# Optimization experiments

Measured on AMD Instinct MI355X. Metric: run time of the kernel, lower is better.

## Reference

```python
import jax, jax.numpy as jnp
import numpy as np

N = 100_000   # nodes
E = 1_600_000 # edges (avg degree 16)
B = 512       # graphs in batch
F_IN = 64; H = 4; D = 64; HD = H * D; EXTRA = 16
NEG_SLOPE = 0.2  # DGL GATConv default


def _gat_conv(x, src, dst, W, al, ar, bias):
    """DGL GATConv: fc -> per-head attn logits -> edge leaky_relu -> segment softmax over dst -> scatter-sum."""
    h = (x @ W).reshape(N, H, D)                       # [N,H,D]
    el = jnp.sum(h * al, axis=-1)                      # [N,H]
    er = jnp.sum(h * ar, axis=-1)                      # [N,H]
    e = jax.nn.leaky_relu(el[src] + er[dst], NEG_SLOPE)  # [E,H]
    m = jax.ops.segment_max(e, dst, num_segments=N)    # [N,H]
    m = jnp.where(jnp.isfinite(m), m, 0.0)             # guard empty segments
    ex = jnp.exp(e - m[dst])                           # [E,H]
    den = jax.ops.segment_sum(ex, dst, num_segments=N) # [N,H]
    alpha = ex / jnp.maximum(den[dst], 1e-9)           # [E,H]
    msg = h[src] * alpha[:, :, None]                   # [E,H,D]
    out = jax.ops.segment_sum(msg, dst, num_segments=N) + bias.reshape(1, H, D)
    return out  # [N,H,D]


def setup_inputs() -> dict:
    key = jax.random.key(0)
    ks = jax.random.split(key, 26)
    nrm = lambda k, shape: jax.random.normal(k, shape, dtype=jnp.float32) * 0.5
    src = jax.random.randint(ks[0], (E,), 0, N)
    # ensure every node has >=1 incoming edge (DGL disallows zero in-degree by default)
    dst = jnp.concatenate([jnp.arange(N), jax.random.randint(ks[1], (E - N,), 0, N)])
    node_graph = jnp.sort(jax.random.randint(ks[2], (N,), 0, B))
    inp = dict(
        src=src, dst=dst, node_graph=node_graph,
        feats_node=jax.random.normal(ks[3], (N, F_IN), dtype=jnp.float32),
        feats_graph=jax.random.normal(ks[4], (B, EXTRA), dtype=jnp.float32),
        W1=nrm(ks[5], (F_IN, HD)), al1=nrm(ks[6], (H, D)), ar1=nrm(ks[7], (H, D)), bg1=jnp.zeros(HD),
        W2=nrm(ks[8], (HD, HD)),  al2=nrm(ks[9], (H, D)), ar2=nrm(ks[10], (H, D)), bg2=jnp.zeros(HD),
        W3=nrm(ks[11], (HD, HD)), al3=nrm(ks[12], (H, D)), ar3=nrm(ks[13], (H, D)), bg3=jnp.zeros(HD),
        sw=nrm(ks[14], (HD, 1)), sb=jnp.zeros(1),
        lw1=nrm(ks[15], (HD + EXTRA, 2 * D)), lb1=jnp.zeros(2 * D),
        lw2=nrm(ks[16], (2 * D, D)), lb2=jnp.zeros(D),
        lw3=nrm(ks[17], (D, 1)), lb3=jnp.zeros(1),
    )
    return inp


def reference(src, dst, node_graph, feats_node, feats_graph,
              W1, al1, ar1, bg1, W2, al2, ar2, bg2, W3, al3, ar3, bg3,
              sw, sb, lw1, lb1, lw2, lb2, lw3, lb3):
    selu = jax.nn.selu
    x = selu(_gat_conv(feats_node, src, dst, W1, al1, ar1, bg1)).reshape(N, HD)
    x = selu(_gat_conv(x, src, dst, W2, al2, ar2, bg2)).reshape(N, HD)
    x = selu(_gat_conv(x, src, dst, W3, al3, ar3, bg3)).reshape(N, HD)
    # WeightedAverage readout: sigmoid-scored weighted mean per graph
    w = jax.nn.sigmoid(x @ sw + sb)                               # [N,1]
    num = jax.ops.segment_sum(w * x, node_graph, num_segments=B)  # [B,HD]
    den = jax.ops.segment_sum(w, node_graph, num_segments=B)      # [B,1]
    emb = num / jnp.maximum(den, 1e-9)
    y = jnp.concatenate([emb, feats_graph], axis=1)
    y = selu(y @ lw1 + lb1)
    y = selu(y @ lw2 + lb2)
    return y @ lw3 + lb3  # [B,1]
```

## Files before the change

kernel.cpp:

```cpp
#include <hip/hip_runtime.h>

#define N_NODES 100000
#define N_EDGES 1600000
#define N_GRAPHS 512
#define F_IN 64
#define HD 256
#define EXTRA 16
#define SCAN_BLOCK 512

typedef float f32x4 __attribute__((ext_vector_type(4)));
typedef _Float16 f16x4 __attribute__((ext_vector_type(4)));
typedef _Float16 f16x8 __attribute__((ext_vector_type(8)));

__device__ __forceinline__ float selu_f(float x) {
    const float a = 1.6732632423543772f, sc = 1.0507009873554805f;
    return x > 0.f ? sc * x : sc * a * (__expf(x) - 1.f);
}

__global__ __launch_bounds__(256) void hist_k(const int* __restrict__ dst, int* __restrict__ hist) {
    int j = blockIdx.x * 256 + threadIdx.x;
    if (j < N_EDGES) atomicAdd(&hist[dst[j]], 1);
}

__global__ __launch_bounds__(SCAN_BLOCK) void scan1_k(const int* __restrict__ hist,
                                                      int* __restrict__ row_ptr,
                                                      int* __restrict__ bsums) {
    __shared__ int sm[SCAN_BLOCK];
    int t = threadIdx.x;
    int i = blockIdx.x * SCAN_BLOCK + t;
    int v = (i < N_NODES) ? hist[i] : 0;
    sm[t] = v;
    __syncthreads();
    for (int off = 1; off < SCAN_BLOCK; off <<= 1) {
        int add = (t >= off) ? sm[t - off] : 0;
        __syncthreads();
        sm[t] += add;
        __syncthreads();
    }
    if (i < N_NODES) row_ptr[i] = sm[t] - v;
    if (t == SCAN_BLOCK - 1) bsums[blockIdx.x] = sm[t];
}

__global__ __launch_bounds__(256) void scan23_k(int* __restrict__ row_ptr, const int* __restrict__ bsums,
                                                int* __restrict__ cursor, int nb) {
    __shared__ int bs[256];
    int t = threadIdx.x;
    bs[t] = (t < nb) ? bsums[t] : 0;
    __syncthreads();
    for (int off = 1; off < 256; off <<= 1) {
        int add = (t >= off) ? bs[t - off] : 0;
        __syncthreads();
        bs[t] += add;
        __syncthreads();
    }
    int i = blockIdx.x * 256 + t;
    if (i < N_NODES) {
        int b = i / SCAN_BLOCK;
        int p = b > 0 ? bs[b - 1] : 0;
        int r = row_ptr[i] + p;
        row_ptr[i] = r;
        cursor[i] = r;
    }
    if (i == 0) row_ptr[N_NODES] = N_EDGES;
}

__global__ __launch_bounds__(256) void scatter_k(const int* __restrict__ src,
                                                 const int* __restrict__ dst,
                                                 int* __restrict__ cursor,
                                                 int* __restrict__ csr_src) {
    int j = blockIdx.x * 256 + threadIdx.x;
    if (j < N_EDGES) {
        int r = atomicAdd(&cursor[dst[j]], 1);
        csr_src[r] = src[j];
    }
}

__device__ __forceinline__ void wsplit(const float* __restrict__ W, _Float16* __restrict__ Wh,
                                       _Float16* __restrict__ Wl, int idx, int K) {
    int n = idx / K, k = idx - n * K;
    float w = W[(size_t)k * HD + n];
    _Float16 hi = (_Float16)w;
    Wh[idx] = hi;
    Wl[idx] = (_Float16)(w - (float)hi);
}

__global__ __launch_bounds__(256) void prep_k(const float* __restrict__ W1,
                                              const float* __restrict__ W2,
                                              const float* __restrict__ W3,
                                              _Float16* __restrict__ W1h, _Float16* __restrict__ W1l,
                                              _Float16* __restrict__ W2h, _Float16* __restrict__ W2l,
                                              _Float16* __restrict__ W3h, _Float16* __restrict__ W3l,
                                              const int* __restrict__ node_graph,
                                              int* __restrict__ gstart) {
    int b = blockIdx.x, t = threadIdx.x;
    if (b < 64) {
        wsplit(W1, W1h, W1l, b * 256 + t, F_IN);
    } else if (b < 320) {
        wsplit(W2, W2h, W2l, (b - 64) * 256 + t, HD);
    } else if (b < 576) {
        wsplit(W3, W3h, W3l, (b - 320) * 256 + t, HD);
    } else {
        int g = (b - 576) * 256 + t;
        if (g > N_GRAPHS) return;
        int lo = 0, hi = N_NODES;
        while (lo < hi) {
            int mid = (lo + hi) >> 1;
            if (node_graph[mid] < g) lo = mid + 1; else hi = mid;
        }
        gstart[g] = lo;
    }
}

template <int K, bool F32A>
__global__ __launch_bounds__(256) void gemm_split_k(const void* __restrict__ Aptr,
                                                    const _Float16* __restrict__ Alo_p,
                                                    const _Float16* __restrict__ Bt_hi,
                                                    const _Float16* __restrict__ Bt_lo,
                                                    const float* __restrict__ al,
                                                    const float* __restrict__ ar,
                                                    _Float16* __restrict__ Chi,
                                                    float* __restrict__ el,
                                                    float* __restrict__ er, int M) {
    const int BM = 64, BN = 128, LDP = 40;
    __shared__ union {
        struct {
            _Float16 Ash[BM][LDP];
            _Float16 Asl[BM][LDP];
            _Float16 Bsh[BN][LDP];
            _Float16 Bsl[BN][LDP];
        } s;
        _Float16 ctile[BM][BN];
    } u;
    __shared__ float pl[4][64];
    __shared__ float pr[4][64];
    _Float16 (&Ash)[BM][LDP] = u.s.Ash;
    _Float16 (&Asl)[BM][LDP] = u.s.Asl;
    _Float16 (&Bsh)[BN][LDP] = u.s.Bsh;
    _Float16 (&Bsl)[BN][LDP] = u.s.Bsl;

    int tid = threadIdx.x;
    int w = tid >> 6, lane = tid & 63;
    int q = lane >> 4, l16 = lane & 15;
    int row0 = blockIdx.y * BM, col0 = blockIdx.x * BN;
    f32x4 acc[4][2] = {};

    int ar_ = tid >> 2, ao = (tid & 3) * 8;
    f16x8 rAh, rAl, rBh[2], rBl[2];

    auto load_tile = [&](int k0) {
        int gr = row0 + ar_;
        if constexpr (F32A) {
            const float* A32 = (const float*)Aptr;
            float vv[8] = {};
            if (gr < M) {
                float4 va = *(const float4*)(A32 + (size_t)gr * K + k0 + ao);
                float4 vb = *(const float4*)(A32 + (size_t)gr * K + k0 + ao + 4);
                vv[0] = va.x; vv[1] = va.y; vv[2] = va.z; vv[3] = va.w;
                vv[4] = vb.x; vv[5] = vb.y; vv[6] = vb.z; vv[7] = vb.w;
            }
            f16x8 h, l;
#pragma unroll
            for (int i = 0; i < 8; i++) {
                h[i] = (_Float16)vv[i];
                l[i] = (_Float16)(vv[i] - (float)h[i]);
            }
            rAh = h; rAl = l;
        } else {
            const _Float16* Ahi = (const _Float16*)Aptr;
            f16x8 vh = {}, vl = {};
            if (gr < M) {
                vh = *(const f16x8*)(Ahi + (size_t)gr * K + k0 + ao);
                vl = *(const f16x8*)(Alo_p + (size_t)gr * K + k0 + ao);
            }
            rAh = vh; rAl = vl;
        }
#pragma unroll
        for (int c = 0; c < 2; c++) {
            int cc = tid + c * 256;
            int br = cc >> 2, bo = (cc & 3) * 8;
            int gb = col0 + br;
            rBh[c] = *(const f16x8*)(Bt_hi + (size_t)gb * K + k0 + bo);
            rBl[c] = *(const f16x8*)(Bt_lo + (size_t)gb * K + k0 + bo);
        }
    };
    auto store_tile = [&]() {
        *(f16x8*)&Ash[ar_][ao] = rAh;
        *(f16x8*)&Asl[ar_][ao] = rAl;
#pragma unroll
        for (int c = 0; c < 2; c++) {
            int cc = tid + c * 256;
            int br = cc >> 2, bo = (cc & 3) * 8;
            *(f16x8*)&Bsh[br][bo] = rBh[c];
            *(f16x8*)&Bsl[br][bo] = rBl[c];
        }
    };

    load_tile(0);
    store_tile();
    __syncthreads();

    for (int k0 = 0; k0 < K; k0 += 32) {
        bool more = (k0 + 32) < K;
        if (more) load_tile(k0 + 32);

        f16x8 ah[4], alo2[4], bh[2], bl[2];
#pragma unroll
        for (int mf = 0; mf < 4; mf++) {
            int m = mf * 16 + l16;
            ah[mf] = *(const f16x8*)&Ash[m][q * 8];
            alo2[mf] = *(const f16x8*)&Asl[m][q * 8];
        }
#pragma unroll
        for (int nf = 0; nf < 2; nf++) {
            int n = w * 32 + nf * 16 + l16;
            bh[nf] = *(const f16x8*)&Bsh[n][q * 8];
            bl[nf] = *(const f16x8*)&Bsl[n][q * 8];
        }
#pragma unroll
        for (int mf = 0; mf < 4; mf++)
#pragma unroll
            for (int nf = 0; nf < 2; nf++) {
                acc[mf][nf] = __builtin_amdgcn_mfma_f32_16x16x32_f16(ah[mf], bh[nf], acc[mf][nf], 0, 0, 0);
                acc[mf][nf] = __builtin_amdgcn_mfma_f32_16x16x32_f16(ah[mf], bl[nf], acc[mf][nf], 0, 0, 0);
                acc[mf][nf] = __builtin_amdgcn_mfma_f32_16x16x32_f16(alo2[mf], bh[nf], acc[mf][nf], 0, 0, 0);
            }
        if (more) {
            __syncthreads();
            store_tile();
            __syncthreads();
        }
    }

    __syncthreads();

    const int hh = (col0 >> 6) + (w >> 1);
    float alv[2], arv[2];
#pragma unroll
    for (int nf = 0; nf < 2; nf++) {
        int d = (w & 1) * 32 + nf * 16 + l16;
        alv[nf] = al[hh * 64 + d];
        arv[nf] = ar[hh * 64 + d];
    }
#pragma unroll
    for (int mf = 0; mf < 4; mf++) {
#pragma unroll
        for (int i = 0; i < 4; i++) {
            int rl = mf * 16 + q * 4 + i;
            float e_l = 0.f, e_r = 0.f;
#pragma unroll
            for (int nf = 0; nf < 2; nf++) {
                float v = acc[mf][nf][i];
                u.ctile[rl][w * 32 + nf * 16 + l16] = (_Float16)v;
                e_l = fmaf(v, alv[nf], e_l);
                e_r = fmaf(v, arv[nf], e_r);
            }
#pragma unroll
            for (int off = 1; off < 16; off <<= 1) {
                e_l += __shfl_xor(e_l, off, 64);
                e_r += __shfl_xor(e_r, off, 64);
            }
            if (l16 == 0) {
                pl[w][rl] = e_l;
                pr[w][rl] = e_r;
            }
        }
    }
    __syncthreads();
#pragma unroll
    for (int j = 0; j < 4; j++) {
        int c = tid + j * 256;
        int rr2 = c >> 4, co = (c & 15) * 8;
        int gr = row0 + rr2;
        if (gr < M)
            *(f16x8*)(Chi + (size_t)gr * HD + col0 + co) = *(const f16x8*)&u.ctile[rr2][co];
    }
    int h2 = (tid >> 6) & 1, rr = tid & 63;
    int grow = row0 + rr;
    if (grow < M) {
        if (tid < 128) el[(size_t)grow * 4 + (col0 >> 6) + h2] = pl[2 * h2][rr] + pl[2 * h2 + 1][rr];
        else           er[(size_t)grow * 4 + (col0 >> 6) + h2] = pr[2 * h2][rr] + pr[2 * h2 + 1][rr];
    }
}

template <int OUT>
__global__ __launch_bounds__(256) void gat_aggregate_k(const _Float16* __restrict__ hb,
                                                       const float* __restrict__ el,
                                                       const float* __restrict__ er,
                                                       const int* __restrict__ csr_src,
                                                       const int* __restrict__ row_ptr,
                                                       const float* __restrict__ bias,
                                                       _Float16* __restrict__ xhi,
                                                       _Float16* __restrict__ xlo,
                                                       float* __restrict__ xf32,
                                                       const float* __restrict__ sw,
                                                       const float* __restrict__ sb,
                                                       float* __restrict__ wsc) {
    __shared__ float wlds[4][64][4];
    __shared__ int snlds[4][64];
    int wv = threadIdx.x >> 6;
    int lane = threadIdx.x & 63;
    int v = blockIdx.x * 4 + wv;
    bool valid = v < N_NODES;
    int vc = valid ? v : 0;
    int rs = row_ptr[vc];
    int deg = valid ? row_ptr[vc + 1] - rs : 0;
    float4 erv = make_float4(0.f, 0.f, 0.f, 0.f);
    if (valid) erv = *(const float4*)(er + (size_t)vc * 4);

    int head = lane >> 4;
    float inv_den = 1.f;
    float m_h = 0.f, er_h = 0.f;
    f16x4 hv_pre[8];
    int nb0 = 0;

    if (deg <= 64) {
        float e0 = -1e30f, e1 = -1e30f, e2 = -1e30f, e3 = -1e30f;
        int my_sn = 0;
        if (lane < deg) {
            my_sn = csr_src[rs + lane];
            float4 elv = *(const float4*)(el + (size_t)my_sn * 4);
            float t0 = elv.x + erv.x, t1 = elv.y + erv.y, t2 = elv.z + erv.z, t3 = elv.w + erv.w;
            e0 = t0 > 0.f ? t0 : 0.2f * t0;
            e1 = t1 > 0.f ? t1 : 0.2f * t1;
            e2 = t2 > 0.f ? t2 : 0.2f * t2;
            e3 = t3 > 0.f ? t3 : 0.2f * t3;
        }
        nb0 = deg < 8 ? deg : 8;
#pragma unroll
        for (int u = 0; u < 8; u++) {
            int snb = __shfl(my_sn, u, 64);
            if (u < nb0) hv_pre[u] = *(const f16x4*)(hb + (size_t)snb * HD + lane * 4);
        }
        float m0 = e0, m1 = e1, m2 = e2, m3 = e3;
        for (int off = 1; off < deg; off <<= 1) {
            m0 = fmaxf(m0, __shfl_xor(m0, off, 64));
            m1 = fmaxf(m1, __shfl_xor(m1, off, 64));
            m2 = fmaxf(m2, __shfl_xor(m2, off, 64));
            m3 = fmaxf(m3, __shfl_xor(m3, off, 64));
        }
        float p0 = 0.f, p1 = 0.f, p2 = 0.f, p3 = 0.f;
        if (lane < deg) {
            p0 = __expf(e0 - m0); p1 = __expf(e1 - m1);
            p2 = __expf(e2 - m2); p3 = __expf(e3 - m3);
        }
        float s0 = p0, s1 = p1, s2 = p2, s3 = p3;
        for (int off = 1; off < deg; off <<= 1) {
            s0 += __shfl_xor(s0, off, 64);
            s1 += __shfl_xor(s1, off, 64);
            s2 += __shfl_xor(s2, off, 64);
            s3 += __shfl_xor(s3, off, 64);
        }
        float d0 = __shfl(s0, 0, 64), d1 = __shfl(s1, 0, 64);
        float d2 = __shfl(s2, 0, 64), d3 = __shfl(s3, 0, 64);
        float dh = head == 0 ? d0 : head == 1 ? d1 : head == 2 ? d2 : d3;
        inv_den = 1.f / fmaxf(dh, 1e-9f);
        if (lane < deg) {
            wlds[wv][lane][0] = p0;
            wlds[wv][lane][1] = p1;
            wlds[wv][lane][2] = p2;
            wlds[wv][lane][3] = p3;
            snlds[wv][lane] = my_sn;
        }
    } else {
        float m[4] = {-1e30f, -1e30f, -1e30f, -1e30f};
        float s[4] = {0.f, 0.f, 0.f, 0.f};
        for (int t = lane; t < deg; t += 64) {
            int sn = csr_src[rs + t];
            float4 elv = *(const float4*)(el + (size_t)sn * 4);
            float e[4];
            e[0] = elv.x + erv.x; e[1] = elv.y + erv.y; e[2] = elv.z + erv.z; e[3] = elv.w + erv.w;
#pragma unroll
            for (int hh = 0; hh < 4; hh++) {
                float ev = e[hh] > 0.f ? e[hh] : 0.2f * e[hh];
                float mn = fmaxf(m[hh], ev);
                s[hh] = s[hh] * __expf(m[hh] - mn) + __expf(ev - mn);
                m[hh] = mn;
            }
        }
#pragma unroll
        for (int off = 32; off >= 1; off >>= 1) {
#pragma unroll
            for (int hh = 0; hh < 4; hh++) {
                float mo = __shfl_xor(m[hh], off, 64);
                float so = __shfl_xor(s[hh], off, 64);
                float mn = fmaxf(m[hh], mo);
                s[hh] = s[hh] * __expf(m[hh] - mn) + so * __expf(mo - mn);
                m[hh] = mn;
            }
        }
        m_h = head == 0 ? m[0] : head == 1 ? m[1] : head == 2 ? m[2] : m[3];
        float dh = head == 0 ? s[0] : head == 1 ? s[1] : head == 2 ? s[2] : s[3];
        er_h = head == 0 ? erv.x : head == 1 ? erv.y : head == 2 ? erv.z : erv.w;
        inv_den = 1.f / fmaxf(dh, 1e-9f);
    }

    float a0 = 0.f, a1 = 0.f, a2 = 0.f, a3 = 0.f;
    if (deg <= 64) {
#pragma unroll
        for (int u = 0; u < 8; u++) {
            if (u < nb0) {
                float w = wlds[wv][u][head];
                a0 = fmaf(w, (float)hv_pre[u].x, a0);
                a1 = fmaf(w, (float)hv_pre[u].y, a1);
                a2 = fmaf(w, (float)hv_pre[u].z, a2);
                a3 = fmaf(w, (float)hv_pre[u].w, a3);
            }
        }
        int t = 8;
        for (; t + 8 <= deg; t += 8) {
            int sn[8];
            float w[8];
#pragma unroll
            for (int u = 0; u < 8; u++) {
                sn[u] = snlds[wv][t + u];
                w[u] = wlds[wv][t + u][head];
            }
            f16x4 hv[8];
#pragma unroll
            for (int u = 0; u < 8; u++)
                hv[u] = *(const f16x4*)(hb + (size_t)sn[u] * HD + lane * 4);
#pragma unroll
            for (int u = 0; u < 8; u++) {
                a0 = fmaf(w[u], (float)hv[u].x, a0);
                a1 = fmaf(w[u], (float)hv[u].y, a1);
                a2 = fmaf(w[u], (float)hv[u].z, a2);
                a3 = fmaf(w[u], (float)hv[u].w, a3);
            }
        }
        for (; t < deg; t++) {
            int sn = snlds[wv][t];
            float w = wlds[wv][t][head];
            f16x4 hv = *(const f16x4*)(hb + (size_t)sn * HD + lane * 4);
            a0 = fmaf(w, (float)hv.x, a0);
            a1 = fmaf(w, (float)hv.y, a1);
            a2 = fmaf(w, (float)hv.z, a2);
            a3 = fmaf(w, (float)hv.w, a3);
        }
    } else {
        for (int t = 0; t < deg; t++) {
            int sn = csr_src[rs + t];
            float e = el[(size_t)sn * 4 + head] + er_h;
            e = e > 0.f ? e : 0.2f * e;
            float w = __expf(e - m_h);
            f16x4 hv = *(const f16x4*)(hb + (size_t)sn * HD + lane * 4);
            a0 = fmaf(w, (float)hv.x, a0);
            a1 = fmaf(w, (float)hv.y, a1);
            a2 = fmaf(w, (float)hv.z, a2);
            a3 = fmaf(w, (float)hv.w, a3);
        }
    }
    float4 bv = *(const float4*)(bias + lane * 4);
    float4 o;
    o.x = selu_f(fmaf(a0, inv_den, bv.x));
    o.y = selu_f(fmaf(a1, inv_den, bv.y));
    o.z = selu_f(fmaf(a2, inv_den, bv.z));
    o.w = selu_f(fmaf(a3, inv_den, bv.w));

    if constexpr (OUT == 0) {
        f16x4 oh, ol;
        oh.x = (_Float16)o.x; ol.x = (_Float16)(o.x - (float)oh.x);
        oh.y = (_Float16)o.y; ol.y = (_Float16)(o.y - (float)oh.y);
        oh.z = (_Float16)o.z; ol.z = (_Float16)(o.z - (float)oh.z);
        oh.w = (_Float16)o.w; ol.w = (_Float16)(o.w - (float)oh.w);
        if (valid) {
            *(f16x4*)(xhi + (size_t)v * HD + lane * 4) = oh;
            *(f16x4*)(xlo + (size_t)v * HD + lane * 4) = ol;
        }
    } else {
        if (valid) *(float4*)(xf32 + (size_t)v * HD + lane * 4) = o;
        float4 sv = *(const float4*)(sw + lane * 4);
        float p = o.x * sv.x + o.y * sv.y + o.z * sv.z + o.w * sv.w;
#pragma unroll
        for (int off = 1; off < 64; off <<= 1) p += __shfl_xor(p, off, 64);
        if (lane == 0 && valid) wsc[v] = 1.f / (1.f + __expf(-(p + sb[0])));
    }
}

__global__ __launch_bounds__(256) void readout_part_k(const float* __restrict__ x,
                                                      const float* __restrict__ wsc,
                                                      const int* __restrict__ gstart,
                                                      float* __restrict__ y0p) {
    int g = blockIdx.x >> 2, c = blockIdx.x & 3;
    int f = threadIdx.x;
    int s0 = gstart[g], e0 = gstart[g + 1];
    int len = e0 - s0;
    int cs = s0 + (len * c) / 4, ce = s0 + (len * (c + 1)) / 4;
    float num = 0.f, den = 0.f;
#pragma unroll 4
    for (int n = cs; n < ce; n++) {
        float wn = wsc[n];
        num = fmaf(wn, x[(size_t)n * HD + f], num);
        den += wn;
    }
    float* dst = y0p + (size_t)(g * 4 + c) * 257;
    dst[f] = num;
    if (f == 0) dst[256] = den;
}

__global__ __launch_bounds__(128) void mlp_k(const float* __restrict__ y0p,
                                             const float* __restrict__ fg,
                                             const float* __restrict__ lw1, const float* __restrict__ lb1,
                                             const float* __restrict__ lw2, const float* __restrict__ lb2,
                                             const float* __restrict__ lw3, const float* __restrict__ lb3,
                                             float* __restrict__ out) {
    __shared__ float y0s[272];
    __shared__ float y1s[128];
    int g = blockIdx.x, t = threadIdx.x;
    const float* p0 = y0p + (size_t)(g * 4 + 0) * 257;
    const float* p1 = y0p + (size_t)(g * 4 + 1) * 257;
    const float* p2 = y0p + (size_t)(g * 4 + 2) * 257;
    const float* p3 = y0p + (size_t)(g * 4 + 3) * 257;
    float den = p0[256] + p1[256] + p2[256] + p3[256];
    float invden = 1.f / fmaxf(den, 1e-9f);
    for (int i = t; i < 256; i += 128)
        y0s[i] = (p0[i] + p1[i] + p2[i] + p3[i]) * invden;
    if (t < EXTRA) y0s[256 + t] = fg[g * EXTRA + t];
    __syncthreads();
    float acc = lb1[t];
    for (int k = 0; k < 272; k++) acc = fmaf(y0s[k], lw1[k * 128 + t], acc);
    y1s[t] = selu_f(acc);
    __syncthreads();
    if (t < 64) {
        float a2 = lb2[t];
        for (int k = 0; k < 128; k++) a2 = fmaf(y1s[k], lw2[k * 64 + t], a2);
        float v2 = selu_f(a2);
        float p = v2 * lw3[t];
#pragma unroll
        for (int off = 1; off < 64; off <<= 1) p += __shfl_xor(p, off, 64);
        if (t == 0) out[g] = p + lb3[0];
    }
}

extern "C" void kernel_launch(void* const* d_in, const int* in_sizes, int n_in,
                              void* d_out, int out_size, void* d_ws, size_t ws_size,
                              hipStream_t stream) {
    const int* src = (const int*)d_in[0];
    const int* dst = (const int*)d_in[1];
    const int* node_graph = (const int*)d_in[2];
    const float* feats_node = (const float*)d_in[3];
    const float* feats_graph = (const float*)d_in[4];
    const float* W1 = (const float*)d_in[5];
    const float* al1 = (const float*)d_in[6];
    const float* ar1 = (const float*)d_in[7];
    const float* bg1 = (const float*)d_in[8];
    const float* W2 = (const float*)d_in[9];
    const float* al2 = (const float*)d_in[10];
    const float* ar2 = (const float*)d_in[11];
    const float* bg2 = (const float*)d_in[12];
    const float* W3 = (const float*)d_in[13];
    const float* al3 = (const float*)d_in[14];
    const float* ar3 = (const float*)d_in[15];
    const float* bg3 = (const float*)d_in[16];
    const float* sw = (const float*)d_in[17];
    const float* sb = (const float*)d_in[18];
    const float* lw1 = (const float*)d_in[19];
    const float* lb1 = (const float*)d_in[20];
    const float* lw2 = (const float*)d_in[21];
    const float* lb2 = (const float*)d_in[22];
    const float* lw3 = (const float*)d_in[23];
    const float* lb3 = (const float*)d_in[24];
    float* out = (float*)d_out;

    char* ws = (char*)d_ws;
    size_t off = 0;
    auto alloc = [&](size_t bytes) -> char* {
        char* p = ws + off;
        off += (bytes + 255) & ~(size_t)255;
        return p;
    };
    _Float16* xhi = (_Float16*)alloc((size_t)N_NODES * HD * 2);
    _Float16* xlo = (_Float16*)alloc((size_t)N_NODES * HD * 2);
    float* xf32 = (float*)xhi;
    _Float16* hhi = (_Float16*)alloc((size_t)N_NODES * HD * 2);
    _Float16* W1hi = (_Float16*)alloc((size_t)F_IN * HD * 2);
    _Float16* W1lo = (_Float16*)alloc((size_t)F_IN * HD * 2);
    _Float16* W2hi = (_Float16*)alloc((size_t)HD * HD * 2);
    _Float16* W2lo = (_Float16*)alloc((size_t)HD * HD * 2);
    _Float16* W3hi = (_Float16*)alloc((size_t)HD * HD * 2);
    _Float16* W3lo = (_Float16*)alloc((size_t)HD * HD * 2);
    float* el = (float*)alloc((size_t)N_NODES * 4 * 4);
    float* er = (float*)alloc((size_t)N_NODES * 4 * 4);
    float* wsc = (float*)alloc((size_t)N_NODES * 4);
    float* y0p = (float*)alloc((size_t)N_GRAPHS * 4 * 257 * 4);
    int* hist = (int*)alloc((size_t)N_NODES * 4);
    int* row_ptr = (int*)alloc((size_t)(N_NODES + 1) * 4);
    int* cursor = (int*)alloc((size_t)N_NODES * 4);
    int* csr_src = (int*)alloc((size_t)N_EDGES * 4);
    int* gstart = (int*)alloc((size_t)(N_GRAPHS + 1) * 4);
    int* bsums = (int*)alloc(256 * 4);
    (void)ws_size; (void)in_sizes; (void)n_in; (void)out_size;

    hipMemsetAsync(hist, 0, (size_t)N_NODES * 4, stream);

    hist_k<<<(N_EDGES + 255) / 256, 256, 0, stream>>>(dst, hist);
    int nb = (N_NODES + SCAN_BLOCK - 1) / SCAN_BLOCK;
    scan1_k<<<nb, SCAN_BLOCK, 0, stream>>>(hist, row_ptr, bsums);
    scan23_k<<<(N_NODES + 255) / 256, 256, 0, stream>>>(row_ptr, bsums, cursor, nb);
    scatter_k<<<(N_EDGES + 255) / 256, 256, 0, stream>>>(src, dst, cursor, csr_src);

    prep_k<<<579, 256, 0, stream>>>(W1, W2, W3, W1hi, W1lo, W2hi, W2lo, W3hi, W3lo, node_graph, gstart);

    dim3 ggrid(HD / 128, (N_NODES + 63) / 64);
    int nwb = (N_NODES + 3) / 4;

    gemm_split_k<F_IN, true><<<ggrid, 256, 0, stream>>>((const void*)feats_node, nullptr, W1hi, W1lo, al1, ar1, hhi, el, er, N_NODES);
    gat_aggregate_k<0><<<nwb, 256, 0, stream>>>(hhi, el, er, csr_src, row_ptr, bg1, xhi, xlo, nullptr, nullptr, nullptr, nullptr);
    gemm_split_k<HD, false><<<ggrid, 256, 0, stream>>>((const void*)xhi, xlo, W2hi, W2lo, al2, ar2, hhi, el, er, N_NODES);
    gat_aggregate_k<0><<<nwb, 256, 0, stream>>>(hhi, el, er, csr_src, row_ptr, bg2, xhi, xlo, nullptr, nullptr, nullptr, nullptr);
    gemm_split_k<HD, false><<<ggrid, 256, 0, stream>>>((const void*)xhi, xlo, W3hi, W3lo, al3, ar3, hhi, el, er, N_NODES);
    gat_aggregate_k<1><<<nwb, 256, 0, stream>>>(hhi, el, er, csr_src, row_ptr, bg3, nullptr, nullptr, xf32, sw, sb, wsc);

    readout_part_k<<<N_GRAPHS * 4, 256, 0, stream>>>(xf32, wsc, gstart, y0p);
    mlp_k<<<N_GRAPHS, 128, 0, stream>>>(y0p, feats_graph, lw1, lb1, lw2, lb2, lw3, lb3, out);
}
```

Before: 926.6 us.

## Split wavefront into two edge halves with 16-byte feature gathers

The aggregation kernel now gives each half-wavefront alternate edges, with each lane loading 8 fp16 features (16 bytes) per neighbor instead of 4. The two halves' partial sums are combined with a cross-half shuffle. The softmax denominator is now accumulated alongside the weighted sum instead of through a separate shuffle reduction. This aims to raise memory-level parallelism and use wider loads per gather, at the cost of more registers (8 accumulators) and some padded, clamped loads when degree is odd.

```diff
diff --git a/kernel.cpp b/kernel.cpp
--- a/kernel.cpp
+++ b/kernel.cpp
@@ -307,11 +307,14 @@
     float4 erv = make_float4(0.f, 0.f, 0.f, 0.f);
     if (valid) erv = *(const float4*)(er + (size_t)vc * 4);
 
-    int head = lane >> 4;
-    float inv_den = 1.f;
+    const int eo = lane >> 5;
+    const int fl = lane & 31;
+    const int headf = fl >> 3;
+
+    float a[8] = {};
+    float dw = 0.f;
+    f16x8 hv_pre[4];
     float m_h = 0.f, er_h = 0.f;
-    f16x4 hv_pre[8];
-    int nb0 = 0;
 
     if (deg <= 64) {
         float e0 = -1e30f, e1 = -1e30f, e2 = -1e30f, e3 = -1e30f;
@@ -325,11 +328,12 @@
             e2 = t2 > 0.f ? t2 : 0.2f * t2;
             e3 = t3 > 0.f ? t3 : 0.2f * t3;
         }
-        nb0 = deg < 8 ? deg : 8;
-#pragma unroll
-        for (int u = 0; u < 8; u++) {
-            int snb = __shfl(my_sn, u, 64);
-            if (u < nb0) hv_pre[u] = *(const f16x4*)(hb + (size_t)snb * HD + lane * 4);
+#pragma unroll
+        for (int u = 0; u < 4; u++) {
+            int pidx = 2 * u + eo;
+            int cidx = pidx < deg ? pidx : (deg > 0 ? deg - 1 : 0);
+            int snb = __shfl(my_sn, cidx, 64);
+            hv_pre[u] = *(const f16x8*)(hb + (size_t)snb * HD + fl * 8);
         }
         float m0 = e0, m1 = e1, m2 = e2, m3 = e3;
         for (int off = 1; off < deg; off <<= 1) {
@@ -338,28 +342,52 @@
             m2 = fmaxf(m2, __shfl_xor(m2, off, 64));
             m3 = fmaxf(m3, __shfl_xor(m3, off, 64));
         }
-        float p0 = 0.f, p1 = 0.f, p2 = 0.f, p3 = 0.f;
         if (lane < deg) {
-            p0 = __expf(e0 - m0); p1 = __expf(e1 - m1);
-            p2 = __expf(e2 - m2); p3 = __expf(e3 - m3);
-        }
-        float s0 = p0, s1 = p1, s2 = p2, s3 = p3;
-        for (int off = 1; off < deg; off <<= 1) {
-            s0 += __shfl_xor(s0, off, 64);
-            s1 += __shfl_xor(s1, off, 64);
-            s2 += __shfl_xor(s2, off, 64);
-            s3 += __shfl_xor(s3, off, 64);
-        }
-        float d0 = __shfl(s0, 0, 64), d1 = __shfl(s1, 0, 64);
-        float d2 = __shfl(s2, 0, 64), d3 = __shfl(s3, 0, 64);
-        float dh = head == 0 ? d0 : head == 1 ? d1 : head == 2 ? d2 : d3;
-        inv_den = 1.f / fmaxf(dh, 1e-9f);
-        if (lane < deg) {
-            wlds[wv][lane][0] = p0;
-            wlds[wv][lane][1] = p1;
-            wlds[wv][lane][2] = p2;
-            wlds[wv][lane][3] = p3;
+            wlds[wv][lane][0] = __expf(e0 - m0);
+            wlds[wv][lane][1] = __expf(e1 - m1);
+            wlds[wv][lane][2] = __expf(e2 - m2);
+            wlds[wv][lane][3] = __expf(e3 - m3);
             snlds[wv][lane] = my_sn;
+        }
+
+#pragma unroll
+        for (int u = 0; u < 4; u++) {
+            int idx = 2 * u + eo;
+            float w = (idx < deg) ? wlds[wv][idx][headf] : 0.f;
+            dw += w;
+#pragma unroll
+            for (int i = 0; i < 8; i++) a[i] = fmaf(w, (float)hv_pre[u][i], a[i]);
+        }
+        int t = 8;
+        for (; t + 8 <= deg; t += 8) {
+            int sn_[4];
+            float w_[4];
+#pragma unroll
+            for (int u = 0; u < 4; u++) {
+                int idx = t + 2 * u + eo;
+                sn_[u] = snlds[wv][idx];
+                w_[u] = wlds[wv][idx][headf];
+            }
+            f16x8 hv[4];
+#pragma unroll
+            for (int u = 0; u < 4; u++)
+                hv[u] = *(const f16x8*)(hb + (size_t)sn_[u] * HD + fl * 8);
+#pragma unroll
+            for (int u = 0; u < 4; u++) {
+                dw += w_[u];
+#pragma unroll
+                for (int i = 0; i < 8; i++) a[i] = fmaf(w_[u], (float)hv[u][i], a[i]);
+            }
+        }
+        for (; t < deg; t += 2) {
+            int idx = t + eo;
+            int cidx = idx < deg ? idx : idx - 1;
+            int sn = snlds[wv][cidx];
+            float w = (idx < deg) ? wlds[wv][cidx][headf] : 0.f;
+            f16x8 hv = *(const f16x8*)(hb + (size_t)sn * HD + fl * 8);
+            dw += w;
+#pragma unroll
+            for (int i = 0; i < 8; i++) a[i] = fmaf(w, (float)hv[i], a[i]);
         }
     } else {
         float m[4] = {-1e30f, -1e30f, -1e30f, -1e30f};
@@ -388,88 +416,72 @@
                 m[hh] = mn;
             }
         }
-        m_h = head == 0 ? m[0] : head == 1 ? m[1] : head == 2 ? m[2] : m[3];
-        float dh = head == 0 ? s[0] : head == 1 ? s[1] : head == 2 ? s[2] : s[3];
-        er_h = head == 0 ? erv.x : head == 1 ? erv.y : head == 2 ? erv.z : erv.w;
-        inv_den = 1.f / fmaxf(dh, 1e-9f);
-    }
-
-    float a0 = 0.f, a1 = 0.f, a2 = 0.f, a3 = 0.f;
-    if (deg <= 64) {
-#pragma unroll
-        for (int u = 0; u < 8; u++) {
-            if (u < nb0) {
-                float w = wlds[wv][u][head];
-                a0 = fmaf(w, (float)hv_pre[u].x, a0);
-                a1 = fmaf(w, (float)hv_pre[u].y, a1);
-                a2 = fmaf(w, (float)hv_pre[u].z, a2);
-                a3 = fmaf(w, (float)hv_pre[u].w, a3);
-            }
-        }
-        int t = 8;
-        for (; t + 8 <= deg; t += 8) {
-            int sn[8];
-            float w[8];
-#pragma unroll
-            for (int u = 0; u < 8; u++) {
-                sn[u] = snlds[wv][t + u];
-                w[u] = wlds[wv][t + u][head];
-            }
-            f16x4 hv[8];
-#pragma unroll
-            for (int u = 0; u < 8; u++)
-                hv[u] = *(const f16x4*)(hb + (size_t)sn[u] * HD + lane * 4);
-#pragma unroll
-            for (int u = 0; u < 8; u++) {
-                a0 = fmaf(w[u], (float)hv[u].x, a0);
-                a1 = fmaf(w[u], (float)hv[u].y, a1);
-                a2 = fmaf(w[u], (float)hv[u].z, a2);
-                a3 = fmaf(w[u], (float)hv[u].w, a3);
-            }
-        }
-        for (; t < deg; t++) {
-            int sn = snlds[wv][t];
-            float w = wlds[wv][t][head];
-            f16x4 hv = *(const f16x4*)(hb + (size_t)sn * HD + lane * 4);
-            a0 = fmaf(w, (float)hv.x, a0);
-            a1 = fmaf(w, (float)hv.y, a1);
-            a2 = fmaf(w, (float)hv.z, a2);
-            a3 = fmaf(w, (float)hv.w, a3);
+        m_h = headf == 0 ? m[0] : headf == 1 ? m[1] : headf == 2 ? m[2] : m[3];
+        float dh = headf == 0 ? s[0] : headf == 1 ? s[1] : headf == 2 ? s[2] : s[3];
+        er_h = headf == 0 ? erv.x : headf == 1 ? erv.y : headf == 2 ? erv.z : erv.w;
+        dw = (eo == 0) ? dh : 0.f;
+
+        for (int t = 0; t < deg; t += 2) {
+            int idx = t + eo;
+            int cidx = idx < deg ? idx : idx - 1;
+            int sn = csr_src[rs + cidx];
+            float w = 0.f;
+            if (idx < deg) {
+                float e = el[(size_t)sn * 4 + headf] + er_h;
+                e = e > 0.f ? e : 0.2f * e;
+                w = __expf(e - m_h);
+            }
+            f16x8 hv = *(const f16x8*)(hb + (size_t)sn * HD + fl * 8);
+#pragma unroll
+            for (int i = 0; i < 8; i++) a[i] = fmaf(w, (float)hv[i], a[i]);
+        }
+    }
+
+#pragma unroll
+    for (int i = 0; i < 8; i++) a[i] += __shfl_xor(a[i], 32, 64);
+    dw += __shfl_xor(dw, 32, 64);
+    float inv_den = 1.f / fmaxf(dw, 1e-9f);
+
+    float4 bv0 = *(const float4*)(bias + fl * 8);
+    float4 bv1 = *(const float4*)(bias + fl * 8 + 4);
+    float o[8];
+    o[0] = selu_f(fmaf(a[0], inv_den, bv0.x));
+    o[1] = selu_f(fmaf(a[1], inv_den, bv0.y));
+    o[2] = selu_f(fmaf(a[2], inv_den, bv0.z));
+    o[3] = selu_f(fmaf(a[3], inv_den, bv0.w));
+    o[4] = selu_f(fmaf(a[4], inv_den, bv1.x));
+    o[5] = selu_f(fmaf(a[5], inv_den, bv1.y));
+    o[6] = selu_f(fmaf(a[6], inv_den, bv1.z));
+    o[7] = selu_f(fmaf(a[7], inv_den, bv1.w));
+
+    if constexpr (OUT == 0) {
+        if (valid) {
+            if (eo == 0) {
+                f16x8 oh;
+#pragma unroll
+                for (int i = 0; i < 8; i++) oh[i] = (_Float16)o[i];
+                *(f16x8*)(xhi + (size_t)v * HD + fl * 8) = oh;
+            } else {
+                f16x8 ol;
+#pragma unroll
+                for (int i = 0; i < 8; i++) {
+                    _Float16 hi = (_Float16)o[i];
+                    ol[i] = (_Float16)(o[i] - (float)hi);
+                }
+                *(f16x8*)(xlo + (size_t)v * HD + fl * 8) = ol;
+            }
         }
     } else {
-        for (int t = 0; t < deg; t++) {
-            int sn = csr_src[rs + t];
-            float e = el[(size_t)sn * 4 + head] + er_h;
-            e = e > 0.f ? e : 0.2f * e;
-            float w = __expf(e - m_h);
-            f16x4 hv = *(const f16x4*)(hb + (size_t)sn * HD + lane * 4);
-            a0 = fmaf(w, (float)hv.x, a0);
-            a1 = fmaf(w, (float)hv.y, a1);
-            a2 = fmaf(w, (float)hv.z, a2);
-            a3 = fmaf(w, (float)hv.w, a3);
-        }
-    }
-    float4 bv = *(const float4*)(bias + lane * 4);
-    float4 o;
-    o.x = selu_f(fmaf(a0, inv_den, bv.x));
-    o.y = selu_f(fmaf(a1, inv_den, bv.y));
-    o.z = selu_f(fmaf(a2, inv_den, bv.z));
-    o.w = selu_f(fmaf(a3, inv_den, bv.w));
-
-    if constexpr (OUT == 0) {
-        f16x4 oh, ol;
-        oh.x = (_Float16)o.x; ol.x = (_Float16)(o.x - (float)oh.x);
-        oh.y = (_Float16)o.y; ol.y = (_Float16)(o.y - (float)oh.y);
-        oh.z = (_Float16)o.z; ol.z = (_Float16)(o.z - (float)oh.z);
-        oh.w = (_Float16)o.w; ol.w = (_Float16)(o.w - (float)oh.w);
-        if (valid) {
-            *(f16x4*)(xhi + (size_t)v * HD + lane * 4) = oh;
-            *(f16x4*)(xlo + (size_t)v * HD + lane * 4) = ol;
-        }
-    } else {
-        if (valid) *(float4*)(xf32 + (size_t)v * HD + lane * 4) = o;
-        float4 sv = *(const float4*)(sw + lane * 4);
-        float p = o.x * sv.x + o.y * sv.y + o.z * sv.z + o.w * sv.w;
+        float p;
+        if (eo == 0) {
+            if (valid) *(float4*)(xf32 + (size_t)v * HD + fl * 8) = make_float4(o[0], o[1], o[2], o[3]);
+            float4 sv = *(const float4*)(sw + fl * 8);
+            p = o[0] * sv.x + o[1] * sv.y + o[2] * sv.z + o[3] * sv.w;
+        } else {
+            if (valid) *(float4*)(xf32 + (size_t)v * HD + fl * 8 + 4) = make_float4(o[4], o[5], o[6], o[7]);
+            float4 sv = *(const float4*)(sw + fl * 8 + 4);
+            p = o[4] * sv.x + o[5] * sv.y + o[6] * sv.z + o[7] * sv.w;
+        }
 #pragma unroll
         for (int off = 1; off < 64; off <<= 1) p += __shfl_xor(p, off, 64);
         if (lane == 0 && valid) wsc[v] = 1.f / (1.f + __expf(-(p + sb[0])));
```

New measurement: 915.8 us. No clear change (-1.2%).
